# Kernel optimization log

Hardware: AMD Instinct MI355X
Metric: run time of the kernel (lower is better)

The kernel has to match this reference:

```python
import jax, jax.numpy as jnp
import numpy as np

B, L, V, E, D, OUT = 64, 256, 50000, 512, 512, 3
PAD_IDX = 0
MAX_DIST = 11
NEG_INF = -1e9


def _mlp2(x, W1, b1, W2, b2):
    # Linear -> ReLU -> (Dropout=id) -> Linear -> ReLU -> (Dropout=id)
    h = jax.nn.relu(x @ W1 + b1)
    return jax.nn.relu(h @ W2 + b2)


def _masked_softmax(x, mask):
    return jax.nn.softmax(jnp.where(mask, x, NEG_INF), axis=-1)


def _rel_bias(n, dist_W):
    pos = jnp.arange(n)
    idx = jnp.clip(pos[None, :] - pos[:, None], -MAX_DIST, MAX_DIST) + MAX_DIST
    return dist_W[idx, 0]  # [n, n]


def _self_branch(x, mask, dist_W, Ws1, bs1, Ws2, bs2):
    # DeepDotAttention(x, x): shared MLP then dot scores [B, L, L]
    q = _mlp2(x, Ws1, bs1, Ws2, bs2)
    scores = jnp.einsum('bqd,bkd->bqk', q, q)
    n = x.shape[1]
    scores = scores + _rel_bias(n, dist_W)[None]           # relative-distance bias
    scores = jnp.where(jnp.eye(n, dtype=bool)[None], -jnp.inf, scores)  # mask diagonal
    scores = jnp.where(mask[:, None, :], scores, 0.0)      # zero padded keys (pre-softmax, as original)
    att = _masked_softmax(scores, mask[:, None, :])
    ctx = jnp.einsum('bqk,bkd->bqd', att, x)
    return jnp.concatenate([x, ctx], axis=-1)               # [B, L, 2E]


def setup_inputs() -> dict:
    key = jax.random.key(0)
    ks = jax.random.split(key, 20)

    def xavier(k, shape):
        fan_in, fan_out = shape[0], shape[1]
        lim = float(np.sqrt(6.0 / (fan_in + fan_out)))
        return jax.random.uniform(k, shape, jnp.float32, -lim, lim)

    embed_W = jax.random.normal(ks[0], (V, E), jnp.float32) * 0.1
    embed_W = embed_W.at[PAD_IDX].set(0.0)  # padding_idx
    inp = {
        'prem_input': jax.random.randint(ks[1], (B, L), 0, V),
        'hypo_input': jax.random.randint(ks[2], (B, L), 0, V),
        'embed_W': embed_W,
        'dist_W': jax.random.normal(ks[3], (2 * MAX_DIST + 1, 1), jnp.float32),
        # self-attention MLP (inp=E)
        'Ws1': xavier(ks[4], (E, D)), 'bs1': jnp.zeros((D,), jnp.float32),
        'Ws2': xavier(ks[5], (D, D)), 'bs2': jnp.zeros((D,), jnp.float32),
        # inter-attention MLP (inp=2E)
        'Wa1': xavier(ks[6], (2 * E, D)), 'ba1': jnp.zeros((D,), jnp.float32),
        'Wa2': xavier(ks[7], (D, D)), 'ba2': jnp.zeros((D,), jnp.float32),
        # compare MLP (inp=4E)
        'Wc1': xavier(ks[8], (4 * E, D)), 'bc1': jnp.zeros((D,), jnp.float32),
        'Wc2': xavier(ks[9], (D, D)), 'bc2': jnp.zeros((D,), jnp.float32),
        # aggregate MLP (inp=2D)
        'Wg1': xavier(ks[10], (2 * D, D)), 'bg1': jnp.zeros((D,), jnp.float32),
        'Wg2': xavier(ks[11], (D, D)), 'bg2': jnp.zeros((D,), jnp.float32),
        # output (no bias)
        'Wo': xavier(ks[12], (D, OUT)),
    }
    return inp


def reference(prem_input, hypo_input, embed_W, dist_W,
              Ws1, bs1, Ws2, bs2, Wa1, ba1, Wa2, ba2,
              Wc1, bc1, Wc2, bc2, Wg1, bg1, Wg2, bg2, Wo):
    prem_mask = prem_input != PAD_IDX  # [B, Lp]
    hypo_mask = hypo_input != PAD_IDX  # [B, Lh]

    prem = embed_W[prem_input]  # [B, Lp, E]
    hypo = embed_W[hypo_input]  # [B, Lh, E]

    prem = _self_branch(prem, prem_mask, dist_W, Ws1, bs1, Ws2, bs2)  # [B, Lp, 2E]
    hypo = _self_branch(hypo, hypo_mask, dist_W, Ws1, bs1, Ws2, bs2)  # [B, Lh, 2E]

    # inter-sentence DeepDotAttention
    pq = _mlp2(prem, Wa1, ba1, Wa2, ba2)
    hk = _mlp2(hypo, Wa1, ba1, Wa2, ba2)
    z = jnp.einsum('bpd,bhd->bph', pq, hk)  # [B, Lp, Lh]

    prem2hypo = _masked_softmax(z, hypo_mask[:, None, :])
    hypo2prem = _masked_softmax(jnp.swapaxes(z, 1, 2), prem_mask[:, None, :])

    attended_hypo = jnp.einsum('bph,bhd->bpd', prem2hypo, hypo)
    attended_prem = jnp.einsum('bhp,bpd->bhd', hypo2prem, prem)

    prem_cmp = _mlp2(jnp.concatenate([prem, attended_hypo], -1), Wc1, bc1, Wc2, bc2)
    hypo_cmp = _mlp2(jnp.concatenate([hypo, attended_prem], -1), Wc1, bc1, Wc2, bc2)
    prem_cmp = (prem_cmp * prem_mask[..., None].astype(prem_cmp.dtype)).sum(axis=1)
    hypo_cmp = (hypo_cmp * hypo_mask[..., None].astype(hypo_cmp.dtype)).sum(axis=1)

    agg = _mlp2(jnp.concatenate([prem_cmp, hypo_cmp], -1), Wg1, bg1, Wg2, bg2)
    return agg @ Wo  # [B, OUT]
```

## Files before the change

### kernel.cpp

```cpp
#include <hip/hip_runtime.h>
#include <math.h>

#define BB   64
#define LL   256
#define EE   512
#define DD   512
#define BL   (BB * LL)
#define BL2  (2 * BL)
#define MAX_DIST 11

typedef __attribute__((ext_vector_type(8))) short bf16x8;
typedef __attribute__((ext_vector_type(8))) unsigned short u16x8;
typedef __attribute__((ext_vector_type(4))) float f32x4;

__device__ __forceinline__ float bf2f(unsigned short u) {
    union { unsigned int u; float f; } v; v.u = ((unsigned int)u) << 16; return v.f;
}
__device__ __forceinline__ unsigned short f2bf(float f) {
    union { float f; unsigned int u; } v; v.f = f;
    unsigned int r = v.u + 0x7FFF + ((v.u >> 16) & 1);
    return (unsigned short)(r >> 16);
}

#define GLOAD16(g, l)                                                          \
    __builtin_amdgcn_global_load_lds(                                          \
        (const __attribute__((address_space(1))) void*)(g),                    \
        (__attribute__((address_space(3))) void*)(l), 16, 0, 0)

template <int MODE>
__global__ __launch_bounds__(256, 2) void bgemm_kernel(
    const unsigned short* __restrict__ A0, int K0, int lda0, long long bsA0,
    const unsigned short* __restrict__ A1, int lda1, long long bsA1,
    const unsigned short* __restrict__ B, int ldb, long long bsB, int bxor,
    const float* __restrict__ bias,
    void* __restrict__ Cv, int ldc, long long bsC,
    int K, int relu,
    const float* __restrict__ smask, const float* __restrict__ distW,
    int diag, int maskXor,
    float* __restrict__ rout, const float* __restrict__ rmask)
{
    constexpr int BN = 256;
    constexpr int NI = 8;
    __shared__ unsigned short smem[(128 + BN) * 64];
    unsigned short* As = smem;
    unsigned short* Bs = smem + 128 * 64;

    const int tid  = threadIdx.x;
    const int wave = tid >> 6;
    const int lane = tid & 63;
    const int quad = lane >> 4;
    const int l15  = lane & 15;
    const int wm   = (wave >> 1) * 64;
    const int wn   = (wave & 1) * 128;
    const int row0 = blockIdx.x * 128;
    const int col0 = blockIdx.y * BN;
    const int b    = blockIdx.z;

    const unsigned short* A0b = A0 + (long long)b * bsA0;
    const unsigned short* A1b = A1 ? (A1 + (long long)b * bsA1) : nullptr;
    const unsigned short* Bb  = B + (long long)(b ^ bxor) * bsB;

    f32x4 acc[4][NI];
#pragma unroll
    for (int i = 0; i < 4; ++i)
#pragma unroll
        for (int j = 0; j < NI; ++j)
            acc[i][j] = (f32x4){0.f, 0.f, 0.f, 0.f};

    for (int kk = 0; kk < K; kk += 64) {
        const unsigned short* Ap; int lda, kloc;
        if (kk < K0) { Ap = A0b; lda = lda0; kloc = kk; }
        else         { Ap = A1b; lda = lda1; kloc = kk - K0; }
#pragma unroll
        for (int it = 0; it < 4; ++it) {
            const int c   = it * 256 + tid;
            const int row = c >> 3;
            const int kch = (c & 7) ^ (row & 7);
            GLOAD16(Ap + (long long)(row0 + row) * lda + kloc + kch * 8,
                    (char*)As + c * 16);
        }
#pragma unroll
        for (int it = 0; it < 8; ++it) {
            const int c   = it * 256 + tid;
            const int row = c >> 3;
            const int kch = (c & 7) ^ (row & 7);
            GLOAD16(Bb + (long long)(col0 + row) * ldb + kk + kch * 8,
                    (char*)Bs + c * 16);
        }
        __syncthreads();

#pragma unroll
        for (int s = 0; s < 2; ++s) {
            bf16x8 fa[4], fb[NI];
#pragma unroll
            for (int mi = 0; mi < 4; ++mi) {
                const int r = wm + mi * 16 + l15;
                const int slot = (s * 4 + quad) ^ (r & 7);
                fa[mi] = *(const bf16x8*)&As[(r * 8 + slot) * 8];
            }
#pragma unroll
            for (int ni = 0; ni < NI; ++ni) {
                const int r = wn + ni * 16 + l15;
                const int slot = (s * 4 + quad) ^ (r & 7);
                fb[ni] = *(const bf16x8*)&Bs[(r * 8 + slot) * 8];
            }
#pragma unroll
            for (int mi = 0; mi < 4; ++mi)
#pragma unroll
                for (int ni = 0; ni < NI; ++ni)
                    acc[mi][ni] = __builtin_amdgcn_mfma_f32_16x16x32_bf16(
                        fa[mi], fb[ni], acc[mi][ni], 0, 0, 0);
        }
        __syncthreads();
    }

    if constexpr (MODE == 2) {
        float bv[NI];
#pragma unroll
        for (int ni = 0; ni < NI; ++ni)
            bv[ni] = bias[col0 + wn + ni * 16 + l15];
        float mrow[4][4];
#pragma unroll
        for (int mi = 0; mi < 4; ++mi)
#pragma unroll
            for (int r = 0; r < 4; ++r)
                mrow[mi][r] = rmask[row0 + wm + mi * 16 + quad * 4 + r];
        float t[NI];
#pragma unroll
        for (int ni = 0; ni < NI; ++ni) t[ni] = 0.f;
#pragma unroll
        for (int mi = 0; mi < 4; ++mi)
#pragma unroll
            for (int ni = 0; ni < NI; ++ni)
#pragma unroll
                for (int r = 0; r < 4; ++r) {
                    float x = fmaxf(acc[mi][ni][r] + bv[ni], 0.f);
                    t[ni] = fmaf(x, mrow[mi][r], t[ni]);
                }
#pragma unroll
        for (int ni = 0; ni < NI; ++ni) {
            t[ni] += __shfl_xor(t[ni], 16, 64);
            t[ni] += __shfl_xor(t[ni], 32, 64);
        }
        if (quad == 0) {
            const int sb = row0 >> 8;
            const int base = (sb & 63) * 1024 + (sb >> 6) * 512;
#pragma unroll
            for (int ni = 0; ni < NI; ++ni)
                atomicAdd(rout + base + col0 + wn + ni * 16 + l15, t[ni]);
        }
        return;
    }

    float bv[NI];
    if constexpr (MODE == 0) {
#pragma unroll
        for (int ni = 0; ni < NI; ++ni)
            bv[ni] = bias ? bias[col0 + wn + ni * 16 + l15] : 0.f;
    } else {
#pragma unroll
        for (int ni = 0; ni < NI; ++ni) bv[ni] = 0.f;
    }

    if constexpr (MODE == 1) {
        __shared__ float red[4][64];
        const int kb = b ^ maskXor;
        float mk[NI];
#pragma unroll
        for (int ni = 0; ni < NI; ++ni)
            mk[ni] = smask[kb * 256 + wn + ni * 16 + l15];
        float rm[4][4];
#pragma unroll
        for (int mi = 0; mi < 4; ++mi)
#pragma unroll
            for (int r = 0; r < 4; ++r) rm[mi][r] = -INFINITY;
#pragma unroll
        for (int mi = 0; mi < 4; ++mi)
#pragma unroll
            for (int r = 0; r < 4; ++r) {
                const int q = row0 + wm + mi * 16 + quad * 4 + r;
#pragma unroll
                for (int ni = 0; ni < NI; ++ni) {
                    const int j = wn + ni * 16 + l15;
                    float s = acc[mi][ni][r];
                    if (distW) {
                        int d = j - q;
                        d = d > MAX_DIST ? MAX_DIST : (d < -MAX_DIST ? -MAX_DIST : d);
                        s += distW[d + MAX_DIST];
                    }
                    if (diag && j == q) s = -INFINITY;
                    if (mk[ni] == 0.f) s = -1e9f;
                    acc[mi][ni][r] = s;
                    rm[mi][r] = fmaxf(rm[mi][r], s);
                }
            }
#pragma unroll
        for (int mi = 0; mi < 4; ++mi)
#pragma unroll
            for (int r = 0; r < 4; ++r) {
                float v = rm[mi][r];
                v = fmaxf(v, __shfl_xor(v, 1, 64));
                v = fmaxf(v, __shfl_xor(v, 2, 64));
                v = fmaxf(v, __shfl_xor(v, 4, 64));
                v = fmaxf(v, __shfl_xor(v, 8, 64));
                rm[mi][r] = v;
            }
        if (l15 == 0) {
#pragma unroll
            for (int mi = 0; mi < 4; ++mi)
#pragma unroll
                for (int r = 0; r < 4; ++r)
                    red[wave][mi * 16 + quad * 4 + r] = rm[mi][r];
        }
        __syncthreads();
#pragma unroll
        for (int mi = 0; mi < 4; ++mi)
#pragma unroll
            for (int r = 0; r < 4; ++r)
                rm[mi][r] = fmaxf(rm[mi][r],
                                  red[wave ^ 1][mi * 16 + quad * 4 + r]);
        float rs[4][4];
#pragma unroll
        for (int mi = 0; mi < 4; ++mi)
#pragma unroll
            for (int r = 0; r < 4; ++r) rs[mi][r] = 0.f;
#pragma unroll
        for (int mi = 0; mi < 4; ++mi)
#pragma unroll
            for (int ni = 0; ni < NI; ++ni)
#pragma unroll
                for (int r = 0; r < 4; ++r) {
                    float e = __expf(acc[mi][ni][r] - rm[mi][r]);
                    acc[mi][ni][r] = e;
                    rs[mi][r] += e;
                }
#pragma unroll
        for (int mi = 0; mi < 4; ++mi)
#pragma unroll
            for (int r = 0; r < 4; ++r) {
                float v = rs[mi][r];
                v += __shfl_xor(v, 1, 64);
                v += __shfl_xor(v, 2, 64);
                v += __shfl_xor(v, 4, 64);
                v += __shfl_xor(v, 8, 64);
                rs[mi][r] = v;
            }
        __syncthreads();
        if (l15 == 0) {
#pragma unroll
            for (int mi = 0; mi < 4; ++mi)
#pragma unroll
                for (int r = 0; r < 4; ++r)
                    red[wave][mi * 16 + quad * 4 + r] = rs[mi][r];
        }
        __syncthreads();
#pragma unroll
        for (int mi = 0; mi < 4; ++mi)
#pragma unroll
            for (int r = 0; r < 4; ++r) {
                float inv = 1.f / (rs[mi][r] +
                                   red[wave ^ 1][mi * 16 + quad * 4 + r] -
                                   rs[mi][r] * 0.f);
                float tot = rs[mi][r] + red[wave ^ 1][mi * 16 + quad * 4 + r];
                inv = 1.f / tot;
#pragma unroll
                for (int ni = 0; ni < NI; ++ni)
                    acc[mi][ni][r] *= inv;
            }
        __syncthreads();
    }

    {
        float* Ls = (float*)smem;
        constexpr int LSW = 257;
        unsigned short* Cb = (unsigned short*)Cv + (long long)b * bsC;
#pragma unroll
        for (int h = 0; h < 4; ++h) {
            if ((wave >> 1) == (h >> 1)) {
                const int mi0 = (h & 1) * 2;
#pragma unroll
                for (int mm = 0; mm < 2; ++mm) {
#pragma unroll
                    for (int ni = 0; ni < NI; ++ni) {
#pragma unroll
                        for (int r = 0; r < 4; ++r) {
                            float x = acc[mi0 + mm][ni][r] + bv[ni];
                            if (MODE == 0 && relu) x = fmaxf(x, 0.f);
                            Ls[(mm * 16 + quad * 4 + r) * LSW +
                               wn + ni * 16 + l15] = x;
                        }
                    }
                }
            }
            __syncthreads();
#pragma unroll
            for (int it = 0; it < 4; ++it) {
                const int c  = it * 256 + tid;
                const int lr = c >> 5;
                const int cc = (c & 31) * 8;
                const float* src = &Ls[lr * LSW + cc];
                u16x8 u;
#pragma unroll
                for (int j = 0; j < 8; ++j) u[j] = f2bf(src[j]);
                *(u16x8*)(Cb + (long long)(row0 + h * 32 + lr) * ldc +
                          col0 + cc) = u;
            }
            __syncthreads();
        }
    }
}

struct WC6 {
    const float* s[6];
    unsigned short* d[6];
    int K[6];
};
__global__ void wconv6_kernel(WC6 wc)
{
    const int z = blockIdx.z;
    const int K = wc.K[z];
    const int k0 = blockIdx.y * 32;
    if (k0 >= K) return;
    const float* src = wc.s[z];
    unsigned short* dst = wc.d[z];
    __shared__ float tile[32][33];
    const int n0 = blockIdx.x * 32;
#pragma unroll
    for (int i = 0; i < 4; ++i)
        tile[threadIdx.y + i * 8][threadIdx.x] =
            src[(long long)(k0 + threadIdx.y + i * 8) * 512 + n0 + threadIdx.x];
    __syncthreads();
#pragma unroll
    for (int i = 0; i < 4; ++i)
        dst[(long long)(n0 + threadIdx.y + i * 8) * K + k0 + threadIdx.x] =
            f2bf(tile[threadIdx.x][threadIdx.y + i * 8]);
}

__global__ void btrans_kernel(const unsigned short* __restrict__ src, int lds_,
                              unsigned short* __restrict__ dst, int C, int bxor)
{
    __shared__ unsigned short tile[32][33];
    const int bz = blockIdx.z;
    const int bs = bz ^ bxor;
    const int c0 = blockIdx.x * 32, l0 = blockIdx.y * 32;
    const unsigned short* s = src + (long long)bs * 256 * lds_;
    unsigned short* d = dst + (long long)bz * C * 256;
#pragma unroll
    for (int i = 0; i < 4; ++i)
        tile[threadIdx.y + i * 8][threadIdx.x] =
            s[(long long)(l0 + threadIdx.y + i * 8) * lds_ + c0 + threadIdx.x];
    __syncthreads();
#pragma unroll
    for (int i = 0; i < 4; ++i)
        d[(long long)(c0 + threadIdx.y + i * 8) * 256 + l0 + threadIdx.x] =
            tile[threadIdx.x][threadIdx.y + i * 8];
}

__global__ void embed_kernel(const int* __restrict__ prem_tok,
                             const int* __restrict__ hypo_tok,
                             const float* __restrict__ W,
                             unsigned short* __restrict__ cat,
                             float* __restrict__ mask)
{
    const int row = blockIdx.x;
    const int t   = threadIdx.x;
    const int tok = row < BL ? prem_tok[row] : hypo_tok[row - BL];
    if (t == 0) mask[row] = (tok != 0) ? 1.0f : 0.0f;
    float4 v = ((const float4*)(W + (long long)tok * EE))[t];
    ushort4 o;
    o.x = f2bf(v.x); o.y = f2bf(v.y); o.z = f2bf(v.z); o.w = f2bf(v.w);
    ((ushort4*)(cat + (long long)row * 1024))[t] = o;
}

__global__ __launch_bounds__(256) void mlp_par_kernel(
    const float* __restrict__ X, const float* __restrict__ W,
    const float* __restrict__ bias, float* __restrict__ Y, int Kin)
{
    __shared__ float red[4][64];
    const int b  = blockIdx.y;
    const int n  = blockIdx.x * 64 + (threadIdx.x & 63);
    const int ts = threadIdx.x >> 6;
    const int kc = Kin >> 2;
    const float* x = X + (long long)b * Kin + ts * kc;
    const float* w = W + (long long)(ts * kc) * 512 + n;
    float a0 = 0.f, a1 = 0.f;
#pragma unroll 8
    for (int k = 0; k < kc; k += 2) {
        a0 = fmaf(x[k],     w[(long long)k * 512],       a0);
        a1 = fmaf(x[k + 1], w[(long long)(k + 1) * 512], a1);
    }
    red[ts][threadIdx.x & 63] = a0 + a1;
    __syncthreads();
    if (ts == 0) {
        float v = red[0][threadIdx.x] + red[1][threadIdx.x] +
                  red[2][threadIdx.x] + red[3][threadIdx.x] + bias[n];
        Y[b * 512 + n] = fmaxf(v, 0.f);
    }
}

__global__ void out_kernel(const float* __restrict__ G,
                           const float* __restrict__ Wo,
                           float* __restrict__ out)
{
    const int wid  = blockIdx.x * 4 + (threadIdx.x >> 6);
    const int lane = threadIdx.x & 63;
    const int b = wid / 3, o = wid % 3;
    float acc = 0.f;
#pragma unroll
    for (int j = 0; j < 8; ++j) {
        int d = lane + j * 64;
        acc = fmaf(G[b * DD + d], Wo[d * 3 + o], acc);
    }
#pragma unroll
    for (int st = 32; st > 0; st >>= 1)
        acc += __shfl_down(acc, st, 64);
    if (lane == 0) out[wid] = acc;
}

struct GemmArgs {
    const unsigned short *A0, *A1, *B;
    int K0, lda0, lda1, ldb;
    long long bsA0, bsA1, bsB;
    int bxor;
    const float* bias;
    void* C; int ldc; long long bsC;
    int M, N, K, relu, batch;
    const float* smask; const float* distW; int diag; int maskXor;
    float* rout; const float* rmask;
};

template <int MODE>
static inline void bgemm_launch(hipStream_t stream, const GemmArgs& a)
{
    dim3 grid(a.M / 128, a.N / 256, a.batch);
    bgemm_kernel<MODE><<<grid, 256, 0, stream>>>(
        a.A0, a.K0, a.lda0, a.bsA0, a.A1, a.lda1, a.bsA1,
        a.B, a.ldb, a.bsB, a.bxor, a.bias, a.C, a.ldc, a.bsC,
        a.K, a.relu, a.smask, a.distW, a.diag, a.maskXor, a.rout, a.rmask);
}

extern "C" void kernel_launch(void* const* d_in, const int* in_sizes, int n_in,
                              void* d_out, int out_size, void* d_ws, size_t ws_size,
                              hipStream_t stream)
{
    (void)in_sizes; (void)n_in; (void)out_size; (void)ws_size;

    const int*   prem_tok = (const int*)d_in[0];
    const int*   hypo_tok = (const int*)d_in[1];
    const float* embW = (const float*)d_in[2];
    const float* dW   = (const float*)d_in[3];
    const float* Ws1  = (const float*)d_in[4];
    const float* bs1  = (const float*)d_in[5];
    const float* Ws2  = (const float*)d_in[6];
    const float* bs2  = (const float*)d_in[7];
    const float* Wa1  = (const float*)d_in[8];
    const float* ba1  = (const float*)d_in[9];
    const float* Wa2  = (const float*)d_in[10];
    const float* ba2  = (const float*)d_in[11];
    const float* Wc1  = (const float*)d_in[12];
    const float* bc1  = (const float*)d_in[13];
    const float* Wc2  = (const float*)d_in[14];
    const float* bc2  = (const float*)d_in[15];
    const float* Wg1  = (const float*)d_in[16];
    const float* bg1  = (const float*)d_in[17];
    const float* Wg2  = (const float*)d_in[18];
    const float* bg2  = (const float*)d_in[19];
    const float* Wo   = (const float*)d_in[20];
    float* out = (float*)d_out;

    char* ws = (char*)d_ws;
    size_t off = 0;
    auto alloc = [&](size_t bytes) {
        char* p = ws + off; off += (bytes + 255) & ~(size_t)255; return p;
    };
    unsigned short* CAT  = (unsigned short*)alloc((size_t)BL2 * 1024 * 2);
    unsigned short* VTF  = (unsigned short*)alloc((size_t)128 * 1024 * 256 * 2);
    unsigned short* Hb   = (unsigned short*)alloc((size_t)BL2 * 512 * 2);
    unsigned short* Q    = (unsigned short*)alloc((size_t)BL2 * 512 * 2);
    unsigned short* ATT  = (unsigned short*)alloc((size_t)BL2 * 1024 * 2);
    unsigned short* SP   = (unsigned short*)alloc((size_t)128 * LL * LL * 2);
    float*          MASK = (float*)alloc((size_t)BL2 * 4);
    float*          R32  = (float*)alloc((size_t)BB * 1024 * 4);
    float*          H64  = (float*)alloc((size_t)BB * 512 * 4);
    float*          G    = (float*)alloc((size_t)BB * 512 * 4);
    unsigned short* WTs1 = (unsigned short*)alloc((size_t)512 * 512 * 2);
    unsigned short* WTs2 = (unsigned short*)alloc((size_t)512 * 512 * 2);
    unsigned short* WTa1 = (unsigned short*)alloc((size_t)1024 * 512 * 2);
    unsigned short* WTa2 = (unsigned short*)alloc((size_t)512 * 512 * 2);
    unsigned short* WTc1 = (unsigned short*)alloc((size_t)2048 * 512 * 2);
    unsigned short* WTc2 = (unsigned short*)alloc((size_t)512 * 512 * 2);

    const long long bsQ = (long long)LL * DD;
    const long long bsS = (long long)LL * LL;
    const long long bsC = (long long)LL * 1024;

    dim3 tb(32, 8);

    WC6 wc;
    wc.s[0] = Ws1; wc.d[0] = WTs1; wc.K[0] = 512;
    wc.s[1] = Ws2; wc.d[1] = WTs2; wc.K[1] = 512;
    wc.s[2] = Wa1; wc.d[2] = WTa1; wc.K[2] = 1024;
    wc.s[3] = Wa2; wc.d[3] = WTa2; wc.K[3] = 512;
    wc.s[4] = Wc1; wc.d[4] = WTc1; wc.K[4] = 2048;
    wc.s[5] = Wc2; wc.d[5] = WTc2; wc.K[5] = 512;
    wconv6_kernel<<<dim3(16, 64, 6), tb, 0, stream>>>(wc);
    hipMemsetAsync(R32, 0, (size_t)BB * 1024 * 4, stream);

    embed_kernel<<<BL2, 128, 0, stream>>>(prem_tok, hypo_tok, embW, CAT, MASK);

    GemmArgs a = {};

    a = {}; a.A0 = CAT; a.K0 = 512; a.lda0 = 1024; a.B = WTs1; a.ldb = 512;
    a.bias = bs1; a.C = Hb; a.ldc = 512; a.M = BL2; a.N = 512; a.K = 512;
    a.relu = 1; a.batch = 1;
    bgemm_launch<0>(stream, a);
    a = {}; a.A0 = Hb; a.K0 = 512; a.lda0 = 512; a.B = WTs2; a.ldb = 512;
    a.bias = bs2; a.C = Q; a.ldc = 512; a.M = BL2; a.N = 512; a.K = 512;
    a.relu = 1; a.batch = 1;
    bgemm_launch<0>(stream, a);

    btrans_kernel<<<dim3(16, 8, 128), tb, 0, stream>>>(CAT, 1024, VTF, 512, 0);

    a = {}; a.A0 = Q; a.K0 = 512; a.lda0 = 512; a.bsA0 = bsQ;
    a.B = Q; a.ldb = 512; a.bsB = bsQ; a.bxor = 0;
    a.C = SP; a.ldc = 256; a.bsC = bsS; a.M = 256; a.N = 256; a.K = 512;
    a.batch = 128; a.smask = MASK; a.distW = dW; a.diag = 1; a.maskXor = 0;
    bgemm_launch<1>(stream, a);

    a = {}; a.A0 = SP; a.K0 = 256; a.lda0 = 256; a.bsA0 = bsS;
    a.B = VTF; a.ldb = 256; a.bsB = (long long)512 * 256;
    a.C = CAT + 512; a.ldc = 1024; a.bsC = bsC;
    a.M = 256; a.N = 512; a.K = 256; a.batch = 128;
    bgemm_launch<0>(stream, a);

    btrans_kernel<<<dim3(32, 8, 128), tb, 0, stream>>>(CAT, 1024, VTF, 1024, 64);

    a = {}; a.A0 = CAT; a.K0 = 1024; a.lda0 = 1024; a.B = WTa1; a.ldb = 1024;
    a.bias = ba1; a.C = Hb; a.ldc = 512; a.M = BL2; a.N = 512; a.K = 1024;
    a.relu = 1; a.batch = 1;
    bgemm_launch<0>(stream, a);
    a = {}; a.A0 = Hb; a.K0 = 512; a.lda0 = 512; a.B = WTa2; a.ldb = 512;
    a.bias = ba2; a.C = Q; a.ldc = 512; a.M = BL2; a.N = 512; a.K = 512;
    a.relu = 1; a.batch = 1;
    bgemm_launch<0>(stream, a);

    a = {}; a.A0 = Q; a.K0 = 512; a.lda0 = 512; a.bsA0 = bsQ;
    a.B = Q; a.ldb = 512; a.bsB = bsQ; a.bxor = 64;
    a.C = SP; a.ldc = 256; a.bsC = bsS; a.M = 256; a.N = 256; a.K = 512;
    a.batch = 128; a.smask = MASK; a.distW = nullptr; a.diag = 0; a.maskXor = 64;
    bgemm_launch<1>(stream, a);

    a = {}; a.A0 = SP; a.K0 = 256; a.lda0 = 256; a.bsA0 = bsS;
    a.B = VTF; a.ldb = 256; a.bsB = (long long)1024 * 256;
    a.C = ATT; a.ldc = 1024; a.bsC = bsC;
    a.M = 256; a.N = 1024; a.K = 256; a.batch = 128;
    bgemm_launch<0>(stream, a);

    a = {}; a.A0 = CAT; a.K0 = 1024; a.lda0 = 1024;
    a.A1 = ATT; a.lda1 = 1024;
    a.B = WTc1; a.ldb = 2048; a.bias = bc1;
    a.C = Hb; a.ldc = 512; a.M = BL2; a.N = 512; a.K = 2048;
    a.relu = 1; a.batch = 1;
    bgemm_launch<0>(stream, a);

    a = {}; a.A0 = Hb; a.K0 = 512; a.lda0 = 512; a.B = WTc2; a.ldb = 512;
    a.bias = bc2; a.M = BL2; a.N = 512; a.K = 512; a.relu = 1; a.batch = 1;
    a.rout = R32; a.rmask = MASK; a.C = Hb;
    bgemm_launch<2>(stream, a);

    mlp_par_kernel<<<dim3(8, BB), 256, 0, stream>>>(R32, Wg1, bg1, H64, 1024);
    mlp_par_kernel<<<dim3(8, BB), 256, 0, stream>>>(H64, Wg2, bg2, G, 512);
    out_kernel<<<48, 256, 0, stream>>>(G, Wo, out);
}
```

Measured before the change: 630.2 us.

## Fuse transposed context write into GEMM epilogue and merge tail kernels

The context GEMM gets a new MODE 3 epilogue that also writes a transposed copy of its output into VTF. This removes the second standalone transpose pass over CAT, and the next GEMM reads VTF through a batch xor instead. The remaining transpose is rewritten with 64x64 tiles and 16-byte vector loads. The R32 memset is folded into the embed kernel, and the three tail MLP/output kernels become one per-batch kernel. Launches and memory traffic go down, but the 64-block aggregate kernel has little parallelism, and the transposed stores from LDS may hit bank conflicts.

After: 633.3 us. No clear change (+0.5%).

```diff
diff --git a/kernel.cpp b/kernel.cpp
--- a/kernel.cpp
+++ b/kernel.cpp
@@ -37,7 +37,8 @@
     int K, int relu,
     const float* __restrict__ smask, const float* __restrict__ distW,
     int diag, int maskXor,
-    float* __restrict__ rout, const float* __restrict__ rmask)
+    float* __restrict__ rout, const float* __restrict__ rmask,
+    unsigned short* __restrict__ tout, long long tbs)
 {
     constexpr int BN = 256;
     constexpr int NI = 8;
@@ -153,7 +154,7 @@
     }
 
     float bv[NI];
-    if constexpr (MODE == 0) {
+    if constexpr (MODE == 0 || MODE == 3) {
 #pragma unroll
         for (int ni = 0; ni < NI; ++ni)
             bv[ni] = bias ? bias[col0 + wn + ni * 16 + l15] : 0.f;
@@ -258,11 +259,9 @@
         for (int mi = 0; mi < 4; ++mi)
 #pragma unroll
             for (int r = 0; r < 4; ++r) {
-                float inv = 1.f / (rs[mi][r] +
-                                   red[wave ^ 1][mi * 16 + quad * 4 + r] -
-                                   rs[mi][r] * 0.f);
-                float tot = rs[mi][r] + red[wave ^ 1][mi * 16 + quad * 4 + r];
-                inv = 1.f / tot;
+                const float tot = rs[mi][r] +
+                                  red[wave ^ 1][mi * 16 + quad * 4 + r];
+                const float inv = 1.f / tot;
 #pragma unroll
                 for (int ni = 0; ni < NI; ++ni)
                     acc[mi][ni][r] *= inv;
@@ -285,7 +284,8 @@
 #pragma unroll
                         for (int r = 0; r < 4; ++r) {
                             float x = acc[mi0 + mm][ni][r] + bv[ni];
-                            if (MODE == 0 && relu) x = fmaxf(x, 0.f);
+                            if ((MODE == 0 || MODE == 3) && relu)
+                                x = fmaxf(x, 0.f);
                             Ls[(mm * 16 + quad * 4 + r) * LSW +
                                wn + ni * 16 + l15] = x;
                         }
@@ -304,6 +304,21 @@
                 for (int j = 0; j < 8; ++j) u[j] = f2bf(src[j]);
                 *(u16x8*)(Cb + (long long)(row0 + h * 32 + lr) * ldc +
                           col0 + cc) = u;
+            }
+            if constexpr (MODE == 3) {
+#pragma unroll
+                for (int it = 0; it < 4; ++it) {
+                    const int idx = it * 256 + tid;
+                    const int c   = idx >> 2;
+                    const int j0  = (idx & 3) * 8;
+                    u16x8 u;
+#pragma unroll
+                    for (int j = 0; j < 8; ++j)
+                        u[j] = f2bf(Ls[(j0 + j) * LSW + c]);
+                    *(u16x8*)(tout + (long long)b * tbs +
+                              (long long)(col0 + c) * 256 +
+                              row0 + h * 32 + j0) = u;
+                }
             }
             __syncthreads();
         }
@@ -336,85 +351,104 @@
             f2bf(tile[threadIdx.x][threadIdx.y + i * 8]);
 }
 
-__global__ void btrans_kernel(const unsigned short* __restrict__ src, int lds_,
-                              unsigned short* __restrict__ dst, int C, int bxor)
+__global__ __launch_bounds__(256) void btransv_kernel(
+    const unsigned short* __restrict__ CAT, unsigned short* __restrict__ VTF)
 {
-    __shared__ unsigned short tile[32][33];
-    const int bz = blockIdx.z;
-    const int bs = bz ^ bxor;
-    const int c0 = blockIdx.x * 32, l0 = blockIdx.y * 32;
-    const unsigned short* s = src + (long long)bs * 256 * lds_;
-    unsigned short* d = dst + (long long)bz * C * 256;
-#pragma unroll
-    for (int i = 0; i < 4; ++i)
-        tile[threadIdx.y + i * 8][threadIdx.x] =
-            s[(long long)(l0 + threadIdx.y + i * 8) * lds_ + c0 + threadIdx.x];
+    __shared__ unsigned short T[64 * 72];
+    const int s  = blockIdx.z;
+    const int c0 = blockIdx.x * 64;
+    const int l0 = blockIdx.y * 64;
+    const unsigned short* src = CAT + (long long)s * 256 * 1024;
+    unsigned short* dst = VTF + (long long)s * 1024 * 256;
+#pragma unroll
+    for (int it = 0; it < 2; ++it) {
+        const int idx = it * 256 + threadIdx.x;
+        const int l   = idx >> 3;
+        const int ch  = idx & 7;
+        u16x8 v = *(const u16x8*)(src + (long long)(l0 + l) * 1024 +
+                                  c0 + ch * 8);
+        *(u16x8*)&T[l * 72 + ch * 8] = v;
+    }
     __syncthreads();
 #pragma unroll
-    for (int i = 0; i < 4; ++i)
-        d[(long long)(c0 + threadIdx.y + i * 8) * 256 + l0 + threadIdx.x] =
-            tile[threadIdx.x][threadIdx.y + i * 8];
+    for (int it = 0; it < 2; ++it) {
+        const int idx = it * 256 + threadIdx.x;
+        const int c   = idx >> 3;
+        const int ch2 = idx & 7;
+        u16x8 u;
+#pragma unroll
+        for (int j = 0; j < 8; ++j)
+            u[j] = T[(ch2 * 8 + j) * 72 + c];
+        *(u16x8*)(dst + (long long)(c0 + c) * 256 + l0 + ch2 * 8) = u;
+    }
 }
 
 __global__ void embed_kernel(const int* __restrict__ prem_tok,
                              const int* __restrict__ hypo_tok,
                              const float* __restrict__ W,
                              unsigned short* __restrict__ cat,
-                             float* __restrict__ mask)
+                             float* __restrict__ mask,
+                             float* __restrict__ R32)
 {
     const int row = blockIdx.x;
     const int t   = threadIdx.x;
     const int tok = row < BL ? prem_tok[row] : hypo_tok[row - BL];
     if (t == 0) mask[row] = (tok != 0) ? 1.0f : 0.0f;
+    if (row < 64) {
+        float4 z = {0.f, 0.f, 0.f, 0.f};
+        ((float4*)(R32 + row * 1024))[t]       = z;
+        ((float4*)(R32 + row * 1024))[t + 128] = z;
+    }
     float4 v = ((const float4*)(W + (long long)tok * EE))[t];
     ushort4 o;
     o.x = f2bf(v.x); o.y = f2bf(v.y); o.z = f2bf(v.z); o.w = f2bf(v.w);
     ((ushort4*)(cat + (long long)row * 1024))[t] = o;
 }
 
-__global__ __launch_bounds__(256) void mlp_par_kernel(
-    const float* __restrict__ X, const float* __restrict__ W,
-    const float* __restrict__ bias, float* __restrict__ Y, int Kin)
+__global__ __launch_bounds__(512) void agg_kernel(
+    const float* __restrict__ R32,
+    const float* __restrict__ Wg1, const float* __restrict__ bg1,
+    const float* __restrict__ Wg2, const float* __restrict__ bg2,
+    const float* __restrict__ Wo, float* __restrict__ out)
 {
-    __shared__ float red[4][64];
-    const int b  = blockIdx.y;
-    const int n  = blockIdx.x * 64 + (threadIdx.x & 63);
-    const int ts = threadIdx.x >> 6;
-    const int kc = Kin >> 2;
-    const float* x = X + (long long)b * Kin + ts * kc;
-    const float* w = W + (long long)(ts * kc) * 512 + n;
+    __shared__ float buf[1024];
+    const int b = blockIdx.x, n = threadIdx.x;
+    buf[n]       = R32[b * 1024 + n];
+    buf[n + 512] = R32[b * 1024 + n + 512];
+    __syncthreads();
     float a0 = 0.f, a1 = 0.f;
 #pragma unroll 8
-    for (int k = 0; k < kc; k += 2) {
-        a0 = fmaf(x[k],     w[(long long)k * 512],       a0);
-        a1 = fmaf(x[k + 1], w[(long long)(k + 1) * 512], a1);
-    }
-    red[ts][threadIdx.x & 63] = a0 + a1;
+    for (int k = 0; k < 1024; k += 2) {
+        a0 = fmaf(buf[k],     Wg1[(long long)k * 512 + n],       a0);
+        a1 = fmaf(buf[k + 1], Wg1[(long long)(k + 1) * 512 + n], a1);
+    }
+    float h = fmaxf(a0 + a1 + bg1[n], 0.f);
     __syncthreads();
-    if (ts == 0) {
-        float v = red[0][threadIdx.x] + red[1][threadIdx.x] +
-                  red[2][threadIdx.x] + red[3][threadIdx.x] + bias[n];
-        Y[b * 512 + n] = fmaxf(v, 0.f);
-    }
-}
-
-__global__ void out_kernel(const float* __restrict__ G,
-                           const float* __restrict__ Wo,
-                           float* __restrict__ out)
-{
-    const int wid  = blockIdx.x * 4 + (threadIdx.x >> 6);
-    const int lane = threadIdx.x & 63;
-    const int b = wid / 3, o = wid % 3;
-    float acc = 0.f;
-#pragma unroll
-    for (int j = 0; j < 8; ++j) {
-        int d = lane + j * 64;
-        acc = fmaf(G[b * DD + d], Wo[d * 3 + o], acc);
-    }
-#pragma unroll
-    for (int st = 32; st > 0; st >>= 1)
-        acc += __shfl_down(acc, st, 64);
-    if (lane == 0) out[wid] = acc;
+    buf[n] = h;
+    __syncthreads();
+    a0 = 0.f; a1 = 0.f;
+#pragma unroll 8
+    for (int k = 0; k < 512; k += 2) {
+        a0 = fmaf(buf[k],     Wg2[(long long)k * 512 + n],       a0);
+        a1 = fmaf(buf[k + 1], Wg2[(long long)(k + 1) * 512 + n], a1);
+    }
+    float g = fmaxf(a0 + a1 + bg2[n], 0.f);
+    __syncthreads();
+    buf[n] = g;
+    __syncthreads();
+    const int wave = n >> 6, lane = n & 63;
+    if (wave < 3) {
+        float acc = 0.f;
+#pragma unroll
+        for (int j = 0; j < 8; ++j) {
+            int d = lane + j * 64;
+            acc = fmaf(buf[d], Wo[d * 3 + wave], acc);
+        }
+#pragma unroll
+        for (int st = 32; st > 0; st >>= 1)
+            acc += __shfl_down(acc, st, 64);
+        if (lane == 0) out[b * 3 + wave] = acc;
+    }
 }
 
 struct GemmArgs {
@@ -427,6 +461,7 @@
     int M, N, K, relu, batch;
     const float* smask; const float* distW; int diag; int maskXor;
     float* rout; const float* rmask;
+    unsigned short* tout; long long tbs;
 };
 
 template <int MODE>
@@ -436,7 +471,8 @@
     bgemm_kernel<MODE><<<grid, 256, 0, stream>>>(
         a.A0, a.K0, a.lda0, a.bsA0, a.A1, a.lda1, a.bsA1,
         a.B, a.ldb, a.bsB, a.bxor, a.bias, a.C, a.ldc, a.bsC,
-        a.K, a.relu, a.smask, a.distW, a.diag, a.maskXor, a.rout, a.rmask);
+        a.K, a.relu, a.smask, a.distW, a.diag, a.maskXor, a.rout, a.rmask,
+        a.tout, a.tbs);
 }
 
 extern "C" void kernel_launch(void* const* d_in, const int* in_sizes, int n_in,
@@ -481,8 +517,6 @@
     unsigned short* SP   = (unsigned short*)alloc((size_t)128 * LL * LL * 2);
     float*          MASK = (float*)alloc((size_t)BL2 * 4);
     float*          R32  = (float*)alloc((size_t)BB * 1024 * 4);
-    float*          H64  = (float*)alloc((size_t)BB * 512 * 4);
-    float*          G    = (float*)alloc((size_t)BB * 512 * 4);
     unsigned short* WTs1 = (unsigned short*)alloc((size_t)512 * 512 * 2);
     unsigned short* WTs2 = (unsigned short*)alloc((size_t)512 * 512 * 2);
     unsigned short* WTa1 = (unsigned short*)alloc((size_t)1024 * 512 * 2);
@@ -493,6 +527,7 @@
     const long long bsQ = (long long)LL * DD;
     const long long bsS = (long long)LL * LL;
     const long long bsC = (long long)LL * 1024;
+    const long long bsV = (long long)1024 * 256;
 
     dim3 tb(32, 8);
 
@@ -504,9 +539,9 @@
     wc.s[4] = Wc1; wc.d[4] = WTc1; wc.K[4] = 2048;
     wc.s[5] = Wc2; wc.d[5] = WTc2; wc.K[5] = 512;
     wconv6_kernel<<<dim3(16, 64, 6), tb, 0, stream>>>(wc);
-    hipMemsetAsync(R32, 0, (size_t)BB * 1024 * 4, stream);
-
-    embed_kernel<<<BL2, 128, 0, stream>>>(prem_tok, hypo_tok, embW, CAT, MASK);
+
+    embed_kernel<<<BL2, 128, 0, stream>>>(prem_tok, hypo_tok, embW, CAT,
+                                          MASK, R32);
 
     GemmArgs a = {};
 
@@ -519,7 +554,7 @@
     a.relu = 1; a.batch = 1;
     bgemm_launch<0>(stream, a);
 
-    btrans_kernel<<<dim3(16, 8, 128), tb, 0, stream>>>(CAT, 1024, VTF, 512, 0);
+    btransv_kernel<<<dim3(8, 4, 128), 256, 0, stream>>>(CAT, VTF);
 
     a = {}; a.A0 = Q; a.K0 = 512; a.lda0 = 512; a.bsA0 = bsQ;
     a.B = Q; a.ldb = 512; a.bsB = bsQ; a.bxor = 0;
@@ -528,12 +563,11 @@
     bgemm_launch<1>(stream, a);
 
     a = {}; a.A0 = SP; a.K0 = 256; a.lda0 = 256; a.bsA0 = bsS;
-    a.B = VTF; a.ldb = 256; a.bsB = (long long)512 * 256;
+    a.B = VTF; a.ldb = 256; a.bsB = bsV;
     a.C = CAT + 512; a.ldc = 1024; a.bsC = bsC;
     a.M = 256; a.N = 512; a.K = 256; a.batch = 128;
-    bgemm_launch<0>(stream, a);
-
-    btrans_kernel<<<dim3(32, 8, 128), tb, 0, stream>>>(CAT, 1024, VTF, 1024, 64);
+    a.tout = VTF + (size_t)512 * 256; a.tbs = bsV;
+    bgemm_launch<3>(stream, a);
 
     a = {}; a.A0 = CAT; a.K0 = 1024; a.lda0 = 1024; a.B = WTa1; a.ldb = 1024;
     a.bias = ba1; a.C = Hb; a.ldc = 512; a.M = BL2; a.N = 512; a.K = 1024;
@@ -551,7 +585,7 @@
     bgemm_launch<1>(stream, a);
 
     a = {}; a.A0 = SP; a.K0 = 256; a.lda0 = 256; a.bsA0 = bsS;
-    a.B = VTF; a.ldb = 256; a.bsB = (long long)1024 * 256;
+    a.B = VTF; a.ldb = 256; a.bsB = bsV; a.bxor = 64;
     a.C = ATT; a.ldc = 1024; a.bsC = bsC;
     a.M = 256; a.N = 1024; a.K = 256; a.batch = 128;
     bgemm_launch<0>(stream, a);
@@ -568,7 +602,5 @@
     a.rout = R32; a.rmask = MASK; a.C = Hb;
     bgemm_launch<2>(stream, a);
 
-    mlp_par_kernel<<<dim3(8, BB), 256, 0, stream>>>(R32, Wg1, bg1, H64, 1024);
-    mlp_par_kernel<<<dim3(8, BB), 256, 0, stream>>>(H64, Wg2, bg2, G, 512);
-    out_kernel<<<48, 256, 0, stream>>>(G, Wo, out);
-}
+    agg_kernel<<<64, 512, 0, stream>>>(R32, Wg1, bg1, Wg2, bg2, Wo, out);
+}
```
